# Optimization experiments

Hardware: AMD Instinct MI355X
Metric: run time of the kernel (lower is better)

Reference implementation:

```python
import jax, jax.numpy as jnp
import numpy as np

HIDDEN = 1024
HEADS = 16
HEAD_DIM = HIDDEN // HEADS
SCALE = HEAD_DIM ** (-0.5)


def setup_inputs() -> dict:
    key = jax.random.key(0)
    ks = jax.random.split(key, 5)
    B, N, C = 8, 1024, HIDDEN
    x = jax.random.normal(ks[0], (B, N, C), dtype=jnp.float32)
    # torch nn.Linear params: weight [out, in], bias [out]
    w_in = jax.random.normal(ks[1], (3 * C, C), dtype=jnp.float32) * (C ** -0.5)
    b_in = jax.random.normal(ks[2], (3 * C,), dtype=jnp.float32) * 0.02
    w_out = jax.random.normal(ks[3], (C, C), dtype=jnp.float32) * (C ** -0.5)
    b_out = jax.random.normal(ks[4], (C,), dtype=jnp.float32) * 0.02
    return {"x": x, "w_in": w_in, "b_in": b_in, "w_out": w_out, "b_out": b_out}


def reference(x, w_in, b_in, w_out, b_out):
    B, N, C = x.shape
    H, D = HEADS, HEAD_DIM
    # in_proj: [B,N,3C] -> (3,B,H,N,D)
    qkv = x @ w_in.T + b_in
    qkv = qkv.reshape(B, N, 3, H, D).transpose(2, 0, 3, 1, 4)
    q, k, v = qkv[0], qkv[1], qkv[2]
    # attention scores scaled after QK^T (same math as scaling q)
    attn = jnp.einsum("bhnd,bhmd->bhnm", q, k) * SCALE
    attn = jax.nn.softmax(attn, axis=-1)
    out = jnp.einsum("bhnm,bhmd->bhnd", attn, v)  # [B,H,N,D]
    out = out.transpose(0, 2, 1, 3).reshape(B, N, C)
    return out @ w_out.T + b_out
```

## Files before the change

### kernel.cpp

```cpp
#include <hip/hip_runtime.h>


typedef __attribute__((ext_vector_type(8))) __bf16 bf16x8;
typedef __attribute__((ext_vector_type(4))) __bf16 bf16x4;
typedef __attribute__((ext_vector_type(4))) float f32x4;
typedef __attribute__((ext_vector_type(4))) short short4v;

__device__ __forceinline__ f32x4 mfma16(bf16x8 a, bf16x8 b, f32x4 c) {
  return __builtin_amdgcn_mfma_f32_16x16x32_bf16(a, b, c, 0, 0, 0);
}

#if __has_builtin(__builtin_amdgcn_mfma_f32_16x16x16bf16_1k)
__device__ __forceinline__ f32x4 mfma_pv(bf16x4 a, bf16x4 b, f32x4 c) {
  short4v as = __builtin_bit_cast(short4v, a);
  short4v bs = __builtin_bit_cast(short4v, b);
  return __builtin_amdgcn_mfma_f32_16x16x16bf16_1k(as, bs, c, 0, 0, 0);
}
#else
__device__ __forceinline__ f32x4 mfma_pv(bf16x4 a, bf16x4 b, f32x4 c) {
  __bf16 z = (__bf16)0.f;
  bf16x8 a8 = {a[0], a[1], a[2], a[3], z, z, z, z};
  bf16x8 b8 = {b[0], b[1], b[2], b[3], z, z, z, z};
  return mfma16(a8, b8, c);
}
#endif

__device__ __forceinline__ float fexp2(float x) {
#if __has_builtin(__builtin_amdgcn_exp2f)
  return __builtin_amdgcn_exp2f(x);
#else
  return exp2f(x);
#endif
}

typedef __attribute__((address_space(1))) const unsigned int gu32;
typedef __attribute__((address_space(3))) unsigned int lu32;

__device__ __forceinline__ void async16(const void* g, void* l) {
  __builtin_amdgcn_global_load_lds((gu32*)g, (lu32*)l, 16, 0, 0);
}

__global__ __launch_bounds__(256) void cvt_all(const float* __restrict__ x,
                                               __bf16* __restrict__ xb,
                                               const float* __restrict__ wi,
                                               __bf16* __restrict__ wib,
                                               const float* __restrict__ wo,
                                               __bf16* __restrict__ wob) {
  int blk = blockIdx.x;
  const float* in;
  __bf16* out;
  int base;
  if (blk < 4096)      { in = x;  out = xb;  base = 0; }
  else if (blk < 5632) { in = wi; out = wib; base = 4096; }
  else                 { in = wo; out = wob; base = 5632; }
  int i = ((blk - base) * 256 + threadIdx.x) * 8;
  float4 a = *(const float4*)(in + i);
  float4 b = *(const float4*)(in + i + 4);
  bf16x8 o;
  o[0] = (__bf16)a.x; o[1] = (__bf16)a.y; o[2] = (__bf16)a.z; o[3] = (__bf16)a.w;
  o[4] = (__bf16)b.x; o[5] = (__bf16)b.y; o[6] = (__bf16)b.z; o[7] = (__bf16)b.w;
  *(bf16x8*)(out + i) = o;
}

template <bool WRITE_VT>
__global__ __launch_bounds__(512, 4) void gemm1(const __bf16* __restrict__ A,
                                                const __bf16* __restrict__ Bm,
                                                const float* __restrict__ bias,
                                                __bf16* __restrict__ C,
                                                __bf16* __restrict__ vt) {
  __shared__ char lds[49152];
  const int t = threadIdx.x;
  const int wv = t >> 6, lane = t & 63;
  const int q16 = lane & 15, quad = lane >> 4;
  const int wm = wv >> 1, wn = wv & 1;
  const int bid = blockIdx.x;
  const long m0 = (long)(bid & 31) * 256;
  const long n0 = (long)(bid >> 5) * 128;

  const int sr4 = t >> 2;
  const int gc = (t & 3) ^ ((sr4 >> 1) & 3);
  const int ldst = wv * 1024;

  const __bf16* srcA0 = A + (m0 + sr4) * 1024 + gc * 8;
  const __bf16* srcA1 = A + (m0 + 128 + sr4) * 1024 + gc * 8;
  const __bf16* srcB  = Bm + (n0 + sr4) * 1024 + gc * 8;

  const int raB = (wm * 64 + q16) * 64 + ((quad ^ ((q16 >> 1) & 3)) * 16);
  const int rbB = (wn * 64 + q16) * 64 + ((quad ^ ((q16 >> 1) & 3)) * 16);

  f32x4 zero = {0.f, 0.f, 0.f, 0.f};
  f32x4 acc[4][4];
#pragma unroll
  for (int i = 0; i < 4; ++i)
#pragma unroll
    for (int j = 0; j < 4; ++j) acc[i][j] = zero;

  async16(srcA0, lds + ldst);
  async16(srcA1, lds + 8192 + ldst);
  async16(srcB, lds + 16384 + ldst);
  __syncthreads();

  int cur = 0;
#pragma unroll 1
  for (int t32 = 0; t32 < 32; ++t32) {
    char* Ac = lds + cur * 24576;
    char* Bc = Ac + 16384;

    if (t32 < 31) {
      char* S = lds + (cur ^ 1) * 24576;
      const int kt = (t32 + 1) * 32;
      async16(srcA0 + kt, S + ldst);
      async16(srcA1 + kt, S + 8192 + ldst);
      async16(srcB + kt, S + 16384 + ldst);
    }

    bf16x8 af[4], bfr[4];
#pragma unroll
    for (int mi = 0; mi < 4; ++mi)
      af[mi] = *(const bf16x8*)(Ac + raB + mi * 1024);
#pragma unroll
    for (int nj = 0; nj < 4; ++nj)
      bfr[nj] = *(const bf16x8*)(Bc + rbB + nj * 1024);

    __builtin_amdgcn_s_setprio(1);
#pragma unroll
    for (int mi = 0; mi < 4; ++mi)
#pragma unroll
      for (int nj = 0; nj < 4; ++nj)
        acc[mi][nj] = mfma16(af[mi], bfr[nj], acc[mi][nj]);
    __builtin_amdgcn_s_setprio(0);

    __syncthreads();
    cur ^= 1;
  }

  if (WRITE_VT && n0 >= 2048) {
    const int b = (int)(m0 >> 10);
    const int nbase = (int)(m0 & 1023) + wm * 64;
#pragma unroll
    for (int nj = 0; nj < 4; ++nj) {
      int col = (int)n0 + wn * 64 + nj * 16 + q16;
      int cc = col - 2048;
      int h = cc >> 6, d = cc & 63;
      float bs = bias[col];
      __bf16* vrow = vt + (((long)(b * 16 + h)) << 16) + (long)d * 1024;
#pragma unroll
      for (int mi = 0; mi < 4; ++mi) {
        int n = nbase + mi * 16 + quad * 4;
        bf16x4 o;
#pragma unroll
        for (int r = 0; r < 4; ++r) o[r] = (__bf16)(acc[mi][nj][r] + bs);
        *(bf16x4*)(vrow + n) = o;
      }
    }
  } else {
#pragma unroll
    for (int nj = 0; nj < 4; ++nj) {
      long col = n0 + wn * 64 + nj * 16 + q16;
      float bs = bias[col];
#pragma unroll
      for (int mi = 0; mi < 4; ++mi) {
        long rowb = m0 + wm * 64 + mi * 16 + quad * 4;
#pragma unroll
        for (int r = 0; r < 4; ++r) {
          float v = acc[mi][nj][r] + bs;
          C[(rowb + r) * 3072 + col] = (__bf16)v;
        }
      }
    }
  }
}

__global__ __launch_bounds__(512, 2) void gemm2(const __bf16* __restrict__ A,
                                                const __bf16* __restrict__ Bm,
                                                const float* __restrict__ bias,
                                                float* __restrict__ C) {
  __shared__ char lds[98304];
  const int t = threadIdx.x;
  const int wv = t >> 6, lane = t & 63;
  const int q16 = lane & 15, quad = lane >> 4;
  const int wm = wv >> 2, wn = wv & 3;
  const long m0 = (long)blockIdx.x * 128;
  const long n0 = (long)blockIdx.y * 256;

  const int sr = t >> 3;
  const int gc = (t & 7) ^ (sr & 7);
  const int ldst = wv * 1024;

  const __bf16* srcA0 = A + (m0 + sr) * 1024 + gc * 8;
  const __bf16* srcA1 = A + (m0 + 64 + sr) * 1024 + gc * 8;
  const __bf16* srcB0 = Bm + (n0 + sr) * 1024 + gc * 8;
  const __bf16* srcB1 = Bm + (n0 + 64 + sr) * 1024 + gc * 8;
  const __bf16* srcB2 = Bm + (n0 + 128 + sr) * 1024 + gc * 8;
  const __bf16* srcB3 = Bm + (n0 + 192 + sr) * 1024 + gc * 8;

  f32x4 zero = {0.f, 0.f, 0.f, 0.f};
  f32x4 acc[4][4];
#pragma unroll
  for (int i = 0; i < 4; ++i)
#pragma unroll
    for (int j = 0; j < 4; ++j) acc[i][j] = zero;

  async16(srcA0, lds + ldst);
  async16(srcA1, lds + 8192 + ldst);
  async16(srcB0, lds + 16384 + ldst);
  async16(srcB1, lds + 24576 + ldst);
  async16(srcB2, lds + 32768 + ldst);
  async16(srcB3, lds + 40960 + ldst);
  __syncthreads();

  int cur = 0;
#pragma unroll 1
  for (int t16 = 0; t16 < 16; ++t16) {
    char* Ac = lds + cur * 49152;
    char* Bc = Ac + 16384;

    if (t16 < 15) {
      char* S = lds + (cur ^ 1) * 49152;
      const int kt = (t16 + 1) * 64;
      async16(srcA0 + kt, S + ldst);
      async16(srcA1 + kt, S + 8192 + ldst);
      async16(srcB0 + kt, S + 16384 + ldst);
      async16(srcB1 + kt, S + 24576 + ldst);
      async16(srcB2 + kt, S + 32768 + ldst);
      async16(srcB3 + kt, S + 40960 + ldst);
    }

#pragma unroll
    for (int kk = 0; kk < 2; ++kk) {
      bf16x8 af[4], bfr[4];
#pragma unroll
      for (int mi = 0; mi < 4; ++mi) {
        int ra = wm * 64 + mi * 16 + q16;
        af[mi] = *(const bf16x8*)(Ac + ra * 128 + (((kk * 4 + quad) ^ (ra & 7)) * 16));
      }
#pragma unroll
      for (int nj = 0; nj < 4; ++nj) {
        int rb = wn * 64 + nj * 16 + q16;
        bfr[nj] = *(const bf16x8*)(Bc + rb * 128 + (((kk * 4 + quad) ^ (rb & 7)) * 16));
      }
      __builtin_amdgcn_s_setprio(1);
#pragma unroll
      for (int mi = 0; mi < 4; ++mi)
#pragma unroll
        for (int nj = 0; nj < 4; ++nj)
          acc[mi][nj] = mfma16(af[mi], bfr[nj], acc[mi][nj]);
      __builtin_amdgcn_s_setprio(0);
    }

    __syncthreads();
    cur ^= 1;
  }

#pragma unroll
  for (int nj = 0; nj < 4; ++nj) {
    long col = n0 + wn * 64 + nj * 16 + q16;
    float bs = bias[col];
#pragma unroll
    for (int mi = 0; mi < 4; ++mi) {
      long rowb = m0 + wm * 64 + mi * 16 + quad * 4;
#pragma unroll
      for (int r = 0; r < 4; ++r) {
        float v = acc[mi][nj][r] + bs;
        C[(rowb + r) * 1024 + col] = v;
      }
    }
  }
}

__global__ __launch_bounds__(256, 4) void attn_kernel(const __bf16* __restrict__ qkv,
                                                      const __bf16* __restrict__ vt,
                                                      __bf16* __restrict__ ao) {
  __shared__ __bf16 Ks[64 * 64];
  __shared__ __bf16 Vt[64 * 64];
  const int t = threadIdx.x;
  const int wv = t >> 6, lane = t & 63;
  const int q16 = lane & 15, quad = lane >> 4;
  const int bh = blockIdx.x;
  const int b = bh >> 4, h = bh & 15;
  const int q0 = blockIdx.y * 128;
  const long rowbase = (long)b * 1024;

  bf16x8 qf0[2], qf1[2];
#pragma unroll
  for (int qh = 0; qh < 2; ++qh) {
    long qrow = rowbase + q0 + qh * 64 + wv * 16 + q16;
    const __bf16* qp = qkv + qrow * 3072 + h * 64 + quad * 8;
    bf16x8 a = *(const bf16x8*)qp;
    bf16x8 c = *(const bf16x8*)(qp + 32);
#pragma unroll
    for (int j = 0; j < 8; ++j) {
      a[j] = (__bf16)((float)a[j] * 0.18033688f);
      c[j] = (__bf16)((float)c[j] * 0.18033688f);
    }
    qf0[qh] = a;
    qf1[qh] = c;
  }

  f32x4 zero = {0.f, 0.f, 0.f, 0.f};
  f32x4 oacc[2][4];
#pragma unroll
  for (int qh = 0; qh < 2; ++qh)
#pragma unroll
    for (int dt = 0; dt < 4; ++dt) oacc[qh][dt] = zero;
  float lcol0 = 0.f, lcol1 = 0.f;

  char* KsB = (char*)Ks;
  char* VtB = (char*)Vt;
  const int sr = t >> 3;
  const int sgc = (t & 7) ^ (sr & 7);
  const int sw = q16 & 7;

  for (int kv0 = 0; kv0 < 1024; kv0 += 64) {
    __syncthreads();
    const __bf16* kg = qkv + (rowbase + kv0 + sr) * 3072 + 1024 + h * 64 + sgc * 8;
    async16(kg, KsB + wv * 1024);
    async16(kg + (long)32 * 3072, KsB + 4096 + wv * 1024);
    const __bf16* vg = vt + (long)bh * 65536 + (long)sr * 1024 + kv0 + sgc * 8;
    async16(vg, VtB + wv * 1024);
    async16(vg + (long)32 * 1024, VtB + 4096 + wv * 1024);
    __syncthreads();

    f32x4 sacc[2][4];
#pragma unroll
    for (int qh = 0; qh < 2; ++qh)
#pragma unroll
      for (int nt = 0; nt < 4; ++nt) sacc[qh][nt] = zero;
#pragma unroll
    for (int nt = 0; nt < 4; ++nt) {
      int kvr = nt * 16 + q16;
      bf16x8 kf0 = *(const bf16x8*)(KsB + kvr * 128 + ((quad ^ sw) * 16));
      bf16x8 kf1 = *(const bf16x8*)(KsB + kvr * 128 + (((4 + quad) ^ sw) * 16));
#pragma unroll
      for (int qh = 0; qh < 2; ++qh) {
        sacc[qh][nt] = mfma16(kf0, qf0[qh], sacc[qh][nt]);
        sacc[qh][nt] = mfma16(kf1, qf1[qh], sacc[qh][nt]);
      }
    }

    bf16x4 pf[2][4];
#pragma unroll
    for (int qh = 0; qh < 2; ++qh) {
      float lc = 0.f;
#pragma unroll
      for (int nt = 0; nt < 4; ++nt)
#pragma unroll
        for (int r = 0; r < 4; ++r) {
          float p = fexp2(sacc[qh][nt][r]);
          lc += p;
          pf[qh][nt][r] = (__bf16)p;
        }
      if (qh == 0) lcol0 += lc; else lcol1 += lc;
    }

#pragma unroll
    for (int nt = 0; nt < 4; ++nt) {
      int c = ((nt * 2 + (quad >> 1)) ^ sw) * 16 + (quad & 1) * 8;
#pragma unroll
      for (int dt = 0; dt < 4; ++dt) {
        bf16x4 vf = *(const bf16x4*)(VtB + (dt * 16 + q16) * 128 + c);
#pragma unroll
        for (int qh = 0; qh < 2; ++qh)
          oacc[qh][dt] = mfma_pv(pf[qh][nt], vf, oacc[qh][dt]);
      }
    }
  }

#pragma unroll
  for (int qh = 0; qh < 2; ++qh) {
    float lcol = qh == 0 ? lcol0 : lcol1;
    lcol += __shfl_xor(lcol, 16);
    lcol += __shfl_xor(lcol, 32);
    float inv = 1.0f / lcol;
#pragma unroll
    for (int r = 0; r < 4; ++r) {
      float ir = __shfl(inv, quad * 4 + r);
      long orow = rowbase + q0 + qh * 64 + wv * 16 + quad * 4 + r;
#pragma unroll
      for (int dt = 0; dt < 4; ++dt)
        ao[orow * 1024 + h * 64 + dt * 16 + q16] = (__bf16)(oacc[qh][dt][r] * ir);
    }
  }
}

extern "C" void kernel_launch(void* const* d_in, const int* in_sizes, int n_in,
                              void* d_out, int out_size, void* d_ws, size_t ws_size,
                              hipStream_t stream) {
  const float* x     = (const float*)d_in[0];
  const float* w_in  = (const float*)d_in[1];
  const float* b_in  = (const float*)d_in[2];
  const float* w_out = (const float*)d_in[3];
  const float* b_out = (const float*)d_in[4];
  float* out = (float*)d_out;

  char* ws = (char*)d_ws;
  __bf16* xb   = (__bf16*)(ws);
  __bf16* wib  = (__bf16*)(ws + 16777216);
  __bf16* wob  = (__bf16*)(ws + 23068672);
  __bf16* qkvb = (__bf16*)(ws + 25165824);
  __bf16* aob  = (__bf16*)(ws + 75497472);
  __bf16* vtg  = (__bf16*)d_out;

  cvt_all<<<6144, 256, 0, stream>>>(x, xb, w_in, wib, w_out, wob);
  gemm1<true><<<768, 512, 0, stream>>>(xb, wib, b_in, qkvb, vtg);
  attn_kernel<<<dim3(128, 8), 256, 0, stream>>>(qkvb, vtg, aob);
  gemm2<<<dim3(64, 4), 512, 0, stream>>>(aob, wob, b_out, out);
}
```

Before: 221.4 us.

## Enlarge QKV GEMM tile to 256x256 with K=64 staging and interleaved loads

The QKV projection GEMM moves from 256x128 tiles to 256x256 tiles with 128 KB of LDS, a K step of 64 split into two halves, and a 2x4 wave layout where each wave holds 8x4 accumulators. Global-to-LDS copies for the next stage are split across the MFMA phases and guarded by explicit vmcnt waits and raw s_barrier calls. Block IDs are swizzled so that neighbouring blocks share operand tiles in L2. This raises arithmetic intensity and cuts redundant global loads, at the cost of higher register and LDS pressure, lower occupancy (2 blocks per CU), and only 384 blocks to spread over the CUs.

```diff
diff --git a/kernel.cpp b/kernel.cpp
--- a/kernel.cpp
+++ b/kernel.cpp
@@ -63,80 +63,109 @@
 }
 
 template <bool WRITE_VT>
-__global__ __launch_bounds__(512, 4) void gemm1(const __bf16* __restrict__ A,
+__global__ __launch_bounds__(512, 2) void gemm1(const __bf16* __restrict__ A,
                                                 const __bf16* __restrict__ Bm,
                                                 const float* __restrict__ bias,
                                                 __bf16* __restrict__ C,
                                                 __bf16* __restrict__ vt) {
-  __shared__ char lds[49152];
+  __shared__ char lds[131072];
   const int t = threadIdx.x;
   const int wv = t >> 6, lane = t & 63;
   const int q16 = lane & 15, quad = lane >> 4;
-  const int wm = wv >> 1, wn = wv & 1;
+  const int wm = wv >> 2, wn = wv & 3;
   const int bid = blockIdx.x;
-  const long m0 = (long)(bid & 31) * 256;
-  const long n0 = (long)(bid >> 5) * 128;
+  const int swz = (bid & 7) * 48 + (bid >> 3);
+  const long m0 = (long)(swz & 31) * 256;
+  const long n0 = (long)(swz >> 5) * 256;
 
   const int sr4 = t >> 2;
   const int gc = (t & 3) ^ ((sr4 >> 1) & 3);
   const int ldst = wv * 1024;
 
-  const __bf16* srcA0 = A + (m0 + sr4) * 1024 + gc * 8;
-  const __bf16* srcA1 = A + (m0 + 128 + sr4) * 1024 + gc * 8;
-  const __bf16* srcB  = Bm + (n0 + sr4) * 1024 + gc * 8;
-
-  const int raB = (wm * 64 + q16) * 64 + ((quad ^ ((q16 >> 1) & 3)) * 16);
-  const int rbB = (wn * 64 + q16) * 64 + ((quad ^ ((q16 >> 1) & 3)) * 16);
+  const __bf16* sA0 = A + (m0 + sr4) * 1024 + gc * 8;
+  const __bf16* sA1 = A + (m0 + 128 + sr4) * 1024 + gc * 8;
+  const __bf16* sB0 = Bm + (n0 + sr4) * 1024 + gc * 8;
+  const __bf16* sB1 = Bm + (n0 + 128 + sr4) * 1024 + gc * 8;
+
+  const int sw4 = (q16 >> 1) & 3;
+  const int raB = (wm * 128 + q16) * 64 + ((quad ^ sw4) * 16);
+  const int rbB = (wn * 64 + q16) * 64 + ((quad ^ sw4) * 16);
 
   f32x4 zero = {0.f, 0.f, 0.f, 0.f};
-  f32x4 acc[4][4];
-#pragma unroll
-  for (int i = 0; i < 4; ++i)
+  f32x4 acc[8][4];
+#pragma unroll
+  for (int i = 0; i < 8; ++i)
 #pragma unroll
     for (int j = 0; j < 4; ++j) acc[i][j] = zero;
 
-  async16(srcA0, lds + ldst);
-  async16(srcA1, lds + 8192 + ldst);
-  async16(srcB, lds + 16384 + ldst);
+  async16(sA0, lds + ldst);
+  async16(sA1, lds + 8192 + ldst);
+  async16(sA0 + 32, lds + 16384 + ldst);
+  async16(sA1 + 32, lds + 16384 + 8192 + ldst);
+  async16(sB0, lds + 32768 + ldst);
+  async16(sB1, lds + 32768 + 8192 + ldst);
+  async16(sB0 + 32, lds + 49152 + ldst);
+  async16(sB1 + 32, lds + 49152 + 8192 + ldst);
   __syncthreads();
 
-  int cur = 0;
 #pragma unroll 1
-  for (int t32 = 0; t32 < 32; ++t32) {
-    char* Ac = lds + cur * 24576;
-    char* Bc = Ac + 16384;
-
-    if (t32 < 31) {
-      char* S = lds + (cur ^ 1) * 24576;
-      const int kt = (t32 + 1) * 32;
-      async16(srcA0 + kt, S + ldst);
-      async16(srcA1 + kt, S + 8192 + ldst);
-      async16(srcB + kt, S + 16384 + ldst);
-    }
-
-    bf16x8 af[4], bfr[4];
-#pragma unroll
-    for (int mi = 0; mi < 4; ++mi)
-      af[mi] = *(const bf16x8*)(Ac + raB + mi * 1024);
-#pragma unroll
-    for (int nj = 0; nj < 4; ++nj)
-      bfr[nj] = *(const bf16x8*)(Bc + rbB + nj * 1024);
-
-    __builtin_amdgcn_s_setprio(1);
-#pragma unroll
-    for (int mi = 0; mi < 4; ++mi)
-#pragma unroll
-      for (int nj = 0; nj < 4; ++nj)
-        acc[mi][nj] = mfma16(af[mi], bfr[nj], acc[mi][nj]);
-    __builtin_amdgcn_s_setprio(0);
-
-    __syncthreads();
-    cur ^= 1;
+  for (int tt = 0; tt < 16; ++tt) {
+    char* cb = lds + (tt & 1) * 65536;
+    char* nb = lds + ((tt & 1) ^ 1) * 65536;
+    const bool st = tt < 15;
+    const int ktn = (tt + 1) * 64;
+
+#pragma unroll
+    for (int kk = 0; kk < 2; ++kk) {
+      char* ca = cb + kk * 16384;
+      char* cbB = cb + 32768 + kk * 16384;
+      bf16x8 af[8], b0, b1;
+
+      if (st) {
+        async16(sA0 + ktn + kk * 32, nb + kk * 16384 + ldst);
+        async16(sA1 + ktn + kk * 32, nb + kk * 16384 + 8192 + ldst);
+      }
+#pragma unroll
+      for (int mi = 0; mi < 8; ++mi)
+        af[mi] = *(const bf16x8*)(ca + raB + mi * 1024);
+      b0 = *(const bf16x8*)(cbB + rbB);
+      b1 = *(const bf16x8*)(cbB + rbB + 1024);
+      __builtin_amdgcn_s_barrier();
+      __builtin_amdgcn_s_setprio(1);
+#pragma unroll
+      for (int mi = 0; mi < 8; ++mi) {
+        acc[mi][0] = mfma16(af[mi], b0, acc[mi][0]);
+        acc[mi][1] = mfma16(af[mi], b1, acc[mi][1]);
+      }
+      __builtin_amdgcn_s_setprio(0);
+      __builtin_amdgcn_s_barrier();
+
+      if (st) {
+        async16(sB0 + ktn + kk * 32, nb + 32768 + kk * 16384 + ldst);
+        async16(sB1 + ktn + kk * 32, nb + 32768 + kk * 16384 + 8192 + ldst);
+      }
+      b0 = *(const bf16x8*)(cbB + rbB + 2048);
+      b1 = *(const bf16x8*)(cbB + rbB + 3072);
+      __builtin_amdgcn_s_barrier();
+      __builtin_amdgcn_s_setprio(1);
+#pragma unroll
+      for (int mi = 0; mi < 8; ++mi) {
+        acc[mi][2] = mfma16(af[mi], b0, acc[mi][2]);
+        acc[mi][3] = mfma16(af[mi], b1, acc[mi][3]);
+      }
+      __builtin_amdgcn_s_setprio(0);
+      if (st) {
+        asm volatile("s_waitcnt vmcnt(4)" ::: "memory");
+      } else {
+        asm volatile("s_waitcnt vmcnt(0)" ::: "memory");
+      }
+      __builtin_amdgcn_s_barrier();
+    }
   }
 
   if (WRITE_VT && n0 >= 2048) {
     const int b = (int)(m0 >> 10);
-    const int nbase = (int)(m0 & 1023) + wm * 64;
+    const int nbase = (int)(m0 & 1023) + wm * 128;
 #pragma unroll
     for (int nj = 0; nj < 4; ++nj) {
       int col = (int)n0 + wn * 64 + nj * 16 + q16;
@@ -145,7 +174,7 @@
       float bs = bias[col];
       __bf16* vrow = vt + (((long)(b * 16 + h)) << 16) + (long)d * 1024;
 #pragma unroll
-      for (int mi = 0; mi < 4; ++mi) {
+      for (int mi = 0; mi < 8; ++mi) {
         int n = nbase + mi * 16 + quad * 4;
         bf16x4 o;
 #pragma unroll
@@ -159,8 +188,8 @@
       long col = n0 + wn * 64 + nj * 16 + q16;
       float bs = bias[col];
 #pragma unroll
-      for (int mi = 0; mi < 4; ++mi) {
-        long rowb = m0 + wm * 64 + mi * 16 + quad * 4;
+      for (int mi = 0; mi < 8; ++mi) {
+        long rowb = m0 + wm * 128 + mi * 16 + quad * 4;
 #pragma unroll
         for (int r = 0; r < 4; ++r) {
           float v = acc[mi][nj][r] + bs;
@@ -402,7 +431,7 @@
   __bf16* vtg  = (__bf16*)d_out;
 
   cvt_all<<<6144, 256, 0, stream>>>(x, xb, w_in, wib, w_out, wob);
-  gemm1<true><<<768, 512, 0, stream>>>(xb, wib, b_in, qkvb, vtg);
+  gemm1<true><<<384, 512, 0, stream>>>(xb, wib, b_in, qkvb, vtg);
   attn_kernel<<<dim3(128, 8), 256, 0, stream>>>(qkvb, vtg, aob);
   gemm2<<<dim3(64, 4), 512, 0, stream>>>(aob, wob, b_out, out);
 }
```

Result: slower. 237.4 us (+7.2%).

## Double-buffer K/V tiles in LDS to overlap loads with attention compute

Applied to the files above, without the earlier changes.

The attention kernel now keeps two LDS buffers each for K and V^T. While the current KV tile is being used for QK^T, softmax and PV, the next tile is prefetched asynchronously. This drops one of the two barriers per iteration and is meant to hide global-memory latency behind MFMA work. It doubles LDS use per block to 32KB, which may lower occupancy. Correctness relies on the end-of-iteration barrier also waiting for the outstanding async loads.

```diff
diff --git a/kernel.cpp b/kernel.cpp
--- a/kernel.cpp
+++ b/kernel.cpp
@@ -271,8 +271,7 @@
 __global__ __launch_bounds__(256, 4) void attn_kernel(const __bf16* __restrict__ qkv,
                                                       const __bf16* __restrict__ vt,
                                                       __bf16* __restrict__ ao) {
-  __shared__ __bf16 Ks[64 * 64];
-  __shared__ __bf16 Vt[64 * 64];
+  __shared__ char lds[32768];
   const int t = threadIdx.x;
   const int wv = t >> 6, lane = t & 63;
   const int q16 = lane & 15, quad = lane >> 4;
@@ -305,21 +304,34 @@
     for (int dt = 0; dt < 4; ++dt) oacc[qh][dt] = zero;
   float lcol0 = 0.f, lcol1 = 0.f;
 
-  char* KsB = (char*)Ks;
-  char* VtB = (char*)Vt;
   const int sr = t >> 3;
   const int sgc = (t & 7) ^ (sr & 7);
   const int sw = q16 & 7;
 
-  for (int kv0 = 0; kv0 < 1024; kv0 += 64) {
-    __syncthreads();
-    const __bf16* kg = qkv + (rowbase + kv0 + sr) * 3072 + 1024 + h * 64 + sgc * 8;
-    async16(kg, KsB + wv * 1024);
-    async16(kg + (long)32 * 3072, KsB + 4096 + wv * 1024);
-    const __bf16* vg = vt + (long)bh * 65536 + (long)sr * 1024 + kv0 + sgc * 8;
-    async16(vg, VtB + wv * 1024);
-    async16(vg + (long)32 * 1024, VtB + 4096 + wv * 1024);
-    __syncthreads();
+  const __bf16* kbase = qkv + (rowbase + sr) * 3072 + 1024 + h * 64 + sgc * 8;
+  const __bf16* vbase = vt + (long)bh * 65536 + (long)sr * 1024 + sgc * 8;
+
+  async16(kbase, lds + wv * 1024);
+  async16(kbase + (long)32 * 3072, lds + 4096 + wv * 1024);
+  async16(vbase, lds + 16384 + wv * 1024);
+  async16(vbase + (long)32 * 1024, lds + 16384 + 4096 + wv * 1024);
+  __syncthreads();
+
+  int cur = 0;
+#pragma unroll 1
+  for (int it = 0; it < 16; ++it) {
+    char* KsB = lds + cur * 8192;
+    char* VtB = lds + 16384 + cur * 8192;
+
+    if (it < 15) {
+      const long kvn = (long)(it + 1) * 64;
+      char* Kn = lds + (cur ^ 1) * 8192;
+      char* Vn = lds + 16384 + (cur ^ 1) * 8192;
+      async16(kbase + kvn * 3072, Kn + wv * 1024);
+      async16(kbase + (kvn + 32) * 3072, Kn + 4096 + wv * 1024);
+      async16(vbase + kvn, Vn + wv * 1024);
+      async16(vbase + kvn + (long)32 * 1024, Vn + 4096 + wv * 1024);
+    }
 
     f32x4 sacc[2][4];
 #pragma unroll
@@ -364,6 +376,9 @@
           oacc[qh][dt] = mfma_pv(pf[qh][nt], vf, oacc[qh][dt]);
       }
     }
+
+    __syncthreads();
+    cur ^= 1;
   }
 
 #pragma unroll
```

Measured after the change: 225.3 us. Within noise of the previous version (+1.8%).
